# Optimization experiments

Measured on AMD Instinct MI355X. Metric: run time of the kernel, lower is better.

Reference implementation:

```python
import jax, jax.numpy as jnp
import numpy as np

GROUP = 4
ALPHA = 2.0


def sda(x, group=GROUP, alpha=ALPHA):
    # Per row: find FIRST group whose elements are all > 0 -> scale by alpha;
    # find FIRST group whose elements are all < 0 -> zero it. Masks are
    # computed on the original values, then applied.
    B, H = x.shape
    G = H // group
    xg = x.reshape(B, G, group)
    all_pos = jnp.all(xg > 0, axis=-1)            # [B, G]
    all_neg = jnp.all(xg < 0, axis=-1)            # [B, G]
    has_pos = jnp.any(all_pos, axis=-1, keepdims=True)   # [B, 1]
    has_neg = jnp.any(all_neg, axis=-1, keepdims=True)   # [B, 1]
    act_idx = jnp.argmax(all_pos, axis=-1, keepdims=True)    # first True
    inact_idx = jnp.argmax(all_neg, axis=-1, keepdims=True)  # first True
    gids = jnp.arange(G)[None, :]                 # [1, G]
    scale = jnp.ones((B, G), dtype=x.dtype)
    scale = jnp.where(has_pos & (gids == act_idx), jnp.asarray(alpha, x.dtype), scale)
    scale = jnp.where(has_neg & (gids == inact_idx), jnp.asarray(0.0, x.dtype), scale)
    return (xg * scale[:, :, None]).reshape(B, H)


def setup_inputs() -> dict:
    key = jax.random.key(0)
    ks = jax.random.split(key, 7)
    d_in, h1, h2, d_out = 1024, 4096, 4096, 1024
    x = jax.random.normal(ks[0], (8192, d_in), dtype=jnp.float32)
    def lin(kw, kb, fan_in, fan_out):
        bound = 1.0 / np.sqrt(fan_in)
        W = jax.random.uniform(kw, (fan_out, fan_in), jnp.float32, -bound, bound)
        b = jax.random.uniform(kb, (fan_out,), jnp.float32, -bound, bound)
        return W, b
    W1, b1 = lin(ks[1], ks[2], d_in, h1)
    W2, b2 = lin(ks[3], ks[4], h1, h2)
    W3, b3 = lin(ks[5], ks[6], h2, d_out)
    return {"x": x, "W1": W1, "b1": b1, "W2": W2, "b2": b2, "W3": W3, "b3": b3}


def reference(x, W1, b1, W2, b2, W3, b3):
    h = sda(x @ W1.T + b1)
    h = sda(h @ W2.T + b2)
    return h @ W3.T + b3
```

## Files before the change

kernel.cpp:

```cpp
#include <hip/hip_runtime.h>
#include <stdint.h>

using half8 = __attribute__((ext_vector_type(8))) _Float16;
using half4 = __attribute__((ext_vector_type(4))) _Float16;
using f32x4 = __attribute__((ext_vector_type(4))) float;

#define BM 256
#define BN 128
#define BK 32

__device__ __forceinline__ int swz(int row, int kb) {
  return (row << 6) + ((((kb >> 4) ^ ((row >> 1) & 3)) << 4) | (kb & 15));
}

__device__ __forceinline__ int xcd_swz(int bid, int nwg) {
  int cpx = nwg >> 3;
  return (bid & 7) * cpx + (bid >> 3);
}

#define GLD(src, dst)                                                          \
  __builtin_amdgcn_global_load_lds(                                            \
      (const __attribute__((address_space(1))) void*)(src),                    \
      (__attribute__((address_space(3))) void*)(dst), 16, 0, 0)

template <int MODE>
__global__ __launch_bounds__(1024, 4)
void gemm_tri(const _Float16* __restrict__ Ahi, const _Float16* __restrict__ Alo,
              const _Float16* __restrict__ Bhi, const _Float16* __restrict__ Blo,
              const float* __restrict__ bias,
              _Float16* __restrict__ Chi, _Float16* __restrict__ Clo,
              float* __restrict__ Cf, int M, int N, int K, int nbx) {
  constexpr bool LO = (MODE < 2);
  constexpr int AHI = 0;
  constexpr int ALO = 16384;
  constexpr int BHI = LO ? 32768 : 16384;
  constexpr int BLO = 40960;
  constexpr int STG = LO ? 49152 : 24576;
  __shared__ char lds[3 * STG];

  const int tid = threadIdx.x;
  const int sid = xcd_swz(blockIdx.x, gridDim.x);
  const int m0 = (sid / nbx) * BM;
  const int n0 = (sid % nbx) * BN;
  const int wave = tid >> 6, lane = tid & 63;
  const int wm = wave >> 1, wn = wave & 1;
  const int NK = K / BK;

  f32x4 acc_hi[2][4], acc_mid[2][4];
#pragma unroll
  for (int m = 0; m < 2; m++)
#pragma unroll
    for (int n = 0; n < 4; n++) { acc_hi[m][n] = (f32x4)0.0f; acc_mid[m][n] = (f32x4)0.0f; }

  const int srow = tid >> 2;
  const int kx = (tid & 3) ^ ((srow >> 1) & 3);
  const size_t aoff = (size_t)(m0 + srow) * K + kx * 8;
  const int brow = (tid & 511) >> 2;
  const size_t boff = (size_t)(n0 + brow) * K + kx * 8;

  auto STAGE = [&](int buf, int ks) {
    char* sb = lds + buf * STG;
    const size_t ko = (size_t)ks * BK;
    GLD(Ahi + aoff + ko, sb + AHI + (wave << 10));
    if constexpr (LO) {
      GLD(Alo + aoff + ko, sb + ALO + (wave << 10));
      if (wave < 8) GLD(Bhi + boff + ko, sb + BHI + (wave << 10));
      else          GLD(Blo + boff + ko, sb + BLO + ((wave - 8) << 10));
    } else {
      if (wave < 8) GLD(Bhi + boff + ko, sb + BHI + (wave << 10));
    }
  };

  auto COMPUTE = [&](int buf) {
    char* base = lds + buf * STG;
    const int kb = (lane >> 4) << 4;
    const int rl = lane & 15;
    half8 ah[2], al[2], bh[4], bl[4];
#pragma unroll
    for (int mi = 0; mi < 2; mi++) {
      int off = swz(wm * 32 + mi * 16 + rl, kb);
      ah[mi] = *(half8*)(base + AHI + off);
      if constexpr (LO) al[mi] = *(half8*)(base + ALO + off);
    }
#pragma unroll
    for (int ni = 0; ni < 4; ni++) {
      int off = swz(wn * 64 + ni * 16 + rl, kb);
      bh[ni] = *(half8*)(base + BHI + off);
      if constexpr (LO) bl[ni] = *(half8*)(base + BLO + off);
    }
    __builtin_amdgcn_s_setprio(1);
#pragma unroll
    for (int mi = 0; mi < 2; mi++)
#pragma unroll
      for (int ni = 0; ni < 4; ni++) {
        acc_hi[mi][ni] = __builtin_amdgcn_mfma_f32_16x16x32_f16(ah[mi], bh[ni], acc_hi[mi][ni], 0, 0, 0);
        if constexpr (LO) {
          acc_mid[mi][ni] = __builtin_amdgcn_mfma_f32_16x16x32_f16(ah[mi], bl[ni], acc_mid[mi][ni], 0, 0, 0);
          acc_mid[mi][ni] = __builtin_amdgcn_mfma_f32_16x16x32_f16(al[mi], bh[ni], acc_mid[mi][ni], 0, 0, 0);
        }
      }
    __builtin_amdgcn_s_setprio(0);
  };

  STAGE(0, 0);
  STAGE(1, 1);
  int cur = 0;
  for (int ks = 0; ks < NK; ++ks) {
    if (ks + 1 < NK) {
      if constexpr (LO) {
        asm volatile("s_waitcnt vmcnt(3)" ::: "memory");
      } else {
        if (wave < 8) asm volatile("s_waitcnt vmcnt(2)" ::: "memory");
        else          asm volatile("s_waitcnt vmcnt(1)" ::: "memory");
      }
    } else {
      asm volatile("s_waitcnt vmcnt(0)" ::: "memory");
    }
    __builtin_amdgcn_s_barrier();
    if (ks + 2 < NK) {
      int nbuf = cur + 2; if (nbuf >= 3) nbuf -= 3;
      STAGE(nbuf, ks + 2);
    }
    COMPUTE(cur);
    if (++cur == 3) cur = 0;
  }

  const int col_l = lane & 15, rgrp = lane >> 4;
#pragma unroll
  for (int ni = 0; ni < 4; ni++) {
    int col = n0 + wn * 64 + ni * 16 + col_l;
    float bv = bias[col];
#pragma unroll
    for (int mi = 0; mi < 2; mi++) {
      int rowb = m0 + wm * 32 + mi * 16 + rgrp * 4;
#pragma unroll
      for (int i = 0; i < 4; i++) {
        size_t idx = (size_t)(rowb + i) * N + col;
        if constexpr (MODE == 2) {
          Cf[idx] = acc_hi[mi][ni][i] + bv;
        } else {
          float c = acc_hi[mi][ni][i] + acc_mid[mi][ni][i] * (1.0f / 2048.0f) + bv;
          _Float16 hh = (_Float16)c;
          Chi[idx] = hh;
          if constexpr (MODE == 0) Clo[idx] = (_Float16)((c - (float)hh) * 2048.0f);
        }
      }
    }
  }
}

#define SQ_BUF 65536

__global__ __launch_bounds__(1024, 4)
void gemm_sq(const _Float16* __restrict__ Ahi, const _Float16* __restrict__ Bhi,
             const float* __restrict__ bias, _Float16* __restrict__ Chi,
             int M, int N, int K, int nbx) {
  __shared__ char lds[2 * SQ_BUF];
  const int tid = threadIdx.x;
  const int sid = xcd_swz(blockIdx.x, gridDim.x);
  const int m0 = (sid / nbx) * 256;
  const int n0 = (sid % nbx) * 256;
  const int wave = tid >> 6, lane = tid & 63;
  const int wm = wave >> 2, wn = wave & 3;
  const int NE = K / 64;

  f32x4 acc[4][4];
#pragma unroll
  for (int m = 0; m < 4; m++)
#pragma unroll
    for (int n = 0; n < 4; n++) acc[m][n] = (f32x4)0.0f;

  const int srow = tid >> 2;
  const int kx = (tid & 3) ^ ((srow >> 1) & 3);
  const size_t aoff = (size_t)(m0 + srow) * K + kx * 8;
  const size_t boff = (size_t)(n0 + srow) * K + kx * 8;

  const int kb = (lane >> 4) << 4;
  const int rl = lane & 15;
  int aswz[4], bswz[4];
#pragma unroll
  for (int i = 0; i < 4; i++) {
    aswz[i] = swz(wm * 64 + i * 16 + rl, kb);
    bswz[i] = 16384 + swz(wn * 64 + i * 16 + rl, kb);
  }

  auto STAGE_H = [&](int buf, int half, int ks) {
    char* sb = lds + buf * SQ_BUF + half * 32768 + (wave << 10);
    const size_t ko = (size_t)ks * BK;
    GLD(Ahi + aoff + ko, sb);
    GLD(Bhi + boff + ko, sb + 16384);
  };

  auto COMPUTE_H = [&](int buf, int half) {
    char* base = lds + buf * SQ_BUF + half * 32768;
    half8 ah[4], bh[4];
#pragma unroll
    for (int i = 0; i < 4; i++) {
      ah[i] = *(half8*)(base + aswz[i]);
      bh[i] = *(half8*)(base + bswz[i]);
    }
    __builtin_amdgcn_s_setprio(1);
#pragma unroll
    for (int mi = 0; mi < 4; mi++)
#pragma unroll
      for (int ni = 0; ni < 4; ni++)
        acc[mi][ni] = __builtin_amdgcn_mfma_f32_16x16x32_f16(ah[mi], bh[ni], acc[mi][ni], 0, 0, 0);
    __builtin_amdgcn_s_setprio(0);
  };

  STAGE_H(0, 0, 0);
  STAGE_H(0, 1, 1);
  int buf = 0;
  for (int e = 0; e < NE; ++e) {
    asm volatile("s_waitcnt vmcnt(0)" ::: "memory");
    __builtin_amdgcn_s_barrier();
    if (e + 1 < NE) STAGE_H(buf ^ 1, 0, 2 * e + 2);
    COMPUTE_H(buf, 0);
    if (e + 1 < NE) STAGE_H(buf ^ 1, 1, 2 * e + 3);
    COMPUTE_H(buf, 1);
    buf ^= 1;
  }

  const int col_l = lane & 15, rgrp = lane >> 4;
#pragma unroll
  for (int ni = 0; ni < 4; ni++) {
    int col = n0 + wn * 64 + ni * 16 + col_l;
    float bv = bias[col];
#pragma unroll
    for (int mi = 0; mi < 4; mi++) {
      int rowb = m0 + wm * 64 + mi * 16 + rgrp * 4;
#pragma unroll
      for (int i = 0; i < 4; i++)
        Chi[(size_t)(rowb + i) * N + col] = (_Float16)(acc[mi][ni][i] + bv);
    }
  }
}

__global__ __launch_bounds__(256)
void split4_kernel(const float* __restrict__ s0, _Float16* __restrict__ h0,
                   _Float16* __restrict__ l0, size_t n0,
                   const float* __restrict__ s1, _Float16* __restrict__ h1,
                   _Float16* __restrict__ l1, size_t n1,
                   const float* __restrict__ s2, _Float16* __restrict__ h2,
                   size_t n2,
                   const float* __restrict__ s3, _Float16* __restrict__ h3,
                   size_t n3) {
  const size_t tot = n0 + n1 + n2 + n3;
  size_t i = (size_t)blockIdx.x * 256 + threadIdx.x;
  const size_t stride = (size_t)gridDim.x * 256;
  for (; i < tot; i += stride) {
    const float* src; _Float16* hi; _Float16* lo; size_t j = i;
    if (j < n0) { src = s0; hi = h0; lo = l0; }
    else if ((j -= n0) < n1) { src = s1; hi = h1; lo = l1; }
    else if ((j -= n1) < n2) { src = s2; hi = h2; lo = nullptr; }
    else { j -= n2; src = s3; hi = h3; lo = nullptr; }
    float4 q = ((const float4*)src)[j];
    float a[4] = {q.x, q.y, q.z, q.w};
    half4 h, l;
#pragma unroll
    for (int k = 0; k < 4; ++k) {
      _Float16 hh = (_Float16)a[k];
      h[k] = hh;
      l[k] = (_Float16)((a[k] - (float)hh) * 2048.0f);
    }
    ((half4*)hi)[j] = h;
    if (lo) ((half4*)lo)[j] = l;
  }
}

__global__ __launch_bounds__(256)
void sda_fix(_Float16* __restrict__ Zhi, _Float16* __restrict__ Zlo,
             const float* __restrict__ Af,
             const _Float16* __restrict__ Ahi, const _Float16* __restrict__ Alo,
             const float* __restrict__ W, const float* __restrict__ bias,
             int H, int K, float TAU) {
  __shared__ int sPos[4], sNeg[4];
  __shared__ int nFix;
  __shared__ int fixIdx[96];
  __shared__ double sRed[4];
  __shared__ float sVal;
  const int row = blockIdx.x;
  _Float16* zh = Zhi + (size_t)row * H;
  _Float16* zl = Zlo ? Zlo + (size_t)row * H : nullptr;
  const int t = threadIdx.x;

  if (t == 0) nFix = 0;
  __syncthreads();

  float v[16];
  {
    half8 a0 = ((const half8*)zh)[t * 2], a1 = ((const half8*)zh)[t * 2 + 1];
    if (zl) {
      half8 b0 = ((const half8*)zl)[t * 2], b1 = ((const half8*)zl)[t * 2 + 1];
#pragma unroll
      for (int e = 0; e < 8; ++e) {
        v[e]     = (float)a0[e] + (float)b0[e] * (1.0f / 2048.0f);
        v[8 + e] = (float)a1[e] + (float)b1[e] * (1.0f / 2048.0f);
      }
    } else {
#pragma unroll
      for (int e = 0; e < 8; ++e) { v[e] = (float)a0[e]; v[8 + e] = (float)a1[e]; }
    }
  }

  bool cposa[4], pposa[4], cnega[4], pnega[4];
  int firstCpos = 0x7fffffff, firstCneg = 0x7fffffff;
#pragma unroll
  for (int j = 0; j < 4; ++j) {
    float g0 = v[j*4], g1 = v[j*4+1], g2 = v[j*4+2], g3 = v[j*4+3];
    cposa[j] = (g0 >  TAU) & (g1 >  TAU) & (g2 >  TAU) & (g3 >  TAU);
    pposa[j] = (g0 > -TAU) & (g1 > -TAU) & (g2 > -TAU) & (g3 > -TAU);
    cnega[j] = (g0 < -TAU) & (g1 < -TAU) & (g2 < -TAU) & (g3 < -TAU);
    pnega[j] = (g0 <  TAU) & (g1 <  TAU) & (g2 <  TAU) & (g3 <  TAU);
    int gi = (t << 2) + j;
    if (cposa[j] && gi < firstCpos) firstCpos = gi;
    if (cnega[j] && gi < firstCneg) firstCneg = gi;
  }
#pragma unroll
  for (int off = 32; off; off >>= 1) {
    firstCpos = min(firstCpos, __shfl_xor(firstCpos, off));
    firstCneg = min(firstCneg, __shfl_xor(firstCneg, off));
  }
  if ((t & 63) == 0) { sPos[t >> 6] = firstCpos; sNeg[t >> 6] = firstCneg; }
  __syncthreads();
  firstCpos = min(min(sPos[0], sPos[1]), min(sPos[2], sPos[3]));
  firstCneg = min(min(sNeg[0], sNeg[1]), min(sNeg[2], sNeg[3]));
  __syncthreads();

#pragma unroll
  for (int j = 0; j < 4; ++j) {
    int gi = (t << 2) + j;
    bool qual = (pposa[j] && !cposa[j] && gi <= firstCpos) ||
                (pnega[j] && !cnega[j] && gi <= firstCneg);
    if (qual) {
#pragma unroll
      for (int e = 0; e < 4; ++e) {
        if (fabsf(v[j*4+e]) < TAU) {
          int slot = atomicAdd(&nFix, 1);
          if (slot < 96) fixIdx[slot] = gi * 4 + e;
        }
      }
    }
  }
  __syncthreads();
  const int nf = min(nFix, 96);
  unsigned fixmask = 0;
  for (int i = 0; i < nf; ++i) {
    const int col = fixIdx[i];
    double s = 0.0;
    const float* wr = W + (size_t)col * K;
    if (Af) {
      const float* ar = Af + (size_t)row * K;
      for (int k = t; k < K; k += 256) s += (double)ar[k] * (double)wr[k];
    } else {
      const _Float16* ah = Ahi + (size_t)row * K;
      const _Float16* al = Alo + (size_t)row * K;
      for (int k = t; k < K; k += 256)
        s += ((double)(float)ah[k] + (double)(float)al[k] * (1.0 / 2048.0)) * (double)wr[k];
    }
#pragma unroll
    for (int off = 32; off; off >>= 1) s += __shfl_xor(s, off);
    if ((t & 63) == 0) sRed[t >> 6] = s;
    __syncthreads();
    if (t == 0)
      sVal = (float)(sRed[0] + sRed[1] + sRed[2] + sRed[3] + (double)bias[col]);
    __syncthreads();
    if ((col >> 4) == t) { v[col & 15] = sVal; fixmask |= 1u << (col & 15); }
    __syncthreads();
  }

  int fp = 0x7fffffff, fn = 0x7fffffff;
#pragma unroll
  for (int j = 0; j < 4; ++j) {
    bool ap = (v[j*4+0] > 0.f) & (v[j*4+1] > 0.f) & (v[j*4+2] > 0.f) & (v[j*4+3] > 0.f);
    bool an = (v[j*4+0] < 0.f) & (v[j*4+1] < 0.f) & (v[j*4+2] < 0.f) & (v[j*4+3] < 0.f);
    int g = (t << 2) + j;
    if (ap && g < fp) fp = g;
    if (an && g < fn) fn = g;
  }
#pragma unroll
  for (int off = 32; off; off >>= 1) {
    fp = min(fp, __shfl_xor(fp, off));
    fn = min(fn, __shfl_xor(fn, off));
  }
  if ((t & 63) == 0) { sPos[t >> 6] = fp; sNeg[t >> 6] = fn; }
  __syncthreads();
  fp = min(min(sPos[0], sPos[1]), min(sPos[2], sPos[3]));
  fn = min(min(sNeg[0], sNeg[1]), min(sNeg[2], sNeg[3]));
  const int act   = (fp == 0x7fffffff) ? -1 : fp;
  const int inact = (fn == 0x7fffffff) ? -1 : fn;

  unsigned chg = fixmask;
#pragma unroll
  for (int j = 0; j < 4; ++j) {
    int g = (t << 2) + j;
    if (g == act) {
      v[j*4+0] *= 2.f; v[j*4+1] *= 2.f; v[j*4+2] *= 2.f; v[j*4+3] *= 2.f;
      chg |= 0xFu << (j * 4);
    } else if (g == inact) {
      v[j*4+0] = v[j*4+1] = v[j*4+2] = v[j*4+3] = 0.f;
      chg |= 0xFu << (j * 4);
    }
  }
  while (chg) {
    int e = __ffs(chg) - 1; chg &= chg - 1;
    float val = v[e];
    _Float16 hh = (_Float16)val;
    zh[(t << 4) + e] = hh;
    if (zl) zl[(t << 4) + e] = (_Float16)((val - (float)hh) * 2048.0f);
  }
}

extern "C" void kernel_launch(void* const* d_in, const int* in_sizes, int n_in,
                              void* d_out, int out_size, void* d_ws, size_t ws_size,
                              hipStream_t stream) {
  const float* x  = (const float*)d_in[0];
  const float* W1 = (const float*)d_in[1];
  const float* b1 = (const float*)d_in[2];
  const float* W2 = (const float*)d_in[3];
  const float* b2 = (const float*)d_in[4];
  const float* W3 = (const float*)d_in[5];
  const float* b3 = (const float*)d_in[6];
  float* out = (float*)d_out;

  const int M = 8192, H = 4096, DIN = 1024, DOUT = 1024;

  char* w = (char*)d_ws;
  _Float16* Z1hi = (_Float16*)(w + 0);
  _Float16* Z1lo = (_Float16*)(w + ((size_t)64 << 20));
  _Float16* Z2hi = (_Float16*)(w + ((size_t)128 << 20));
  _Float16* W2hi = (_Float16*)(w + ((size_t)192 << 20));
  _Float16* xhi  = (_Float16*)(w + ((size_t)128 << 20));
  _Float16* xlo  = (_Float16*)(w + ((size_t)144 << 20));
  _Float16* W1hi = (_Float16*)(w + ((size_t)160 << 20));
  _Float16* W1lo = (_Float16*)(w + ((size_t)168 << 20));
  _Float16* W3hi = (_Float16*)(w + ((size_t)224 << 20));

  split4_kernel<<<2048, 256, 0, stream>>>(
      x,  xhi,  xlo,  (size_t)(M * DIN) >> 2,
      W1, W1hi, W1lo, (size_t)(H * DIN) >> 2,
      W2, W2hi,       (size_t)((size_t)H * H) >> 2,
      W3, W3hi,       (size_t)(DOUT * H) >> 2);

  gemm_tri<0><<<dim3((H / BN) * (M / BM)), dim3(1024), 0, stream>>>(
      xhi, xlo, W1hi, W1lo, b1, Z1hi, Z1lo, (float*)nullptr, M, H, DIN, H / BN);
  sda_fix<<<M, 256, 0, stream>>>(Z1hi, Z1lo, x, (const _Float16*)nullptr,
                                 (const _Float16*)nullptr, W1, b1, H, DIN, 1e-4f);
  gemm_sq<<<dim3((H / 256) * (M / 256)), dim3(1024), 0, stream>>>(
      Z1hi, W2hi, b2, Z2hi, M, H, H, H / 256);
  sda_fix<<<M, 256, 0, stream>>>(Z2hi, (_Float16*)nullptr, (const float*)nullptr,
                                 Z1hi, Z1lo, W2, b2, H, H, 5e-3f);
  gemm_tri<2><<<dim3((DOUT / BN) * (M / BM)), dim3(1024), 0, stream>>>(
      Z2hi, (const _Float16*)nullptr, W3hi, (const _Float16*)nullptr, b3,
      (_Float16*)nullptr, (_Float16*)nullptr, out, M, DOUT, H, DOUT / BN);
}
```

Before: 613.6 us.

## Load A operands directly from global into registers, stage only B in LDS

Both GEMM kernels stop staging the A tile through LDS. Each wave now loads its own A fragments straight from global memory into registers, and only B goes through LDS. The tri-split kernel drops from triple to double buffering with a full vmcnt(0) wait before every barrier. This cuts LDS footprint and LDS read traffic. In exchange it adds uncoalesced, strided global loads that stall the wave. A is no longer shared across the waves in the N direction (wn), so redundant global traffic rises.

```diff
diff --git a/kernel.cpp b/kernel.cpp
--- a/kernel.cpp
+++ b/kernel.cpp
@@ -31,12 +31,9 @@
               _Float16* __restrict__ Chi, _Float16* __restrict__ Clo,
               float* __restrict__ Cf, int M, int N, int K, int nbx) {
   constexpr bool LO = (MODE < 2);
-  constexpr int AHI = 0;
-  constexpr int ALO = 16384;
-  constexpr int BHI = LO ? 32768 : 16384;
-  constexpr int BLO = 40960;
-  constexpr int STG = LO ? 49152 : 24576;
-  __shared__ char lds[3 * STG];
+  constexpr int BLO = 8192;
+  constexpr int STG = LO ? 16384 : 8192;
+  __shared__ char lds[2 * STG];
 
   const int tid = threadIdx.x;
   const int sid = xcd_swz(blockIdx.x, gridDim.x);
@@ -52,41 +49,48 @@
 #pragma unroll
     for (int n = 0; n < 4; n++) { acc_hi[m][n] = (f32x4)0.0f; acc_mid[m][n] = (f32x4)0.0f; }
 
-  const int srow = tid >> 2;
-  const int kx = (tid & 3) ^ ((srow >> 1) & 3);
-  const size_t aoff = (size_t)(m0 + srow) * K + kx * 8;
   const int brow = (tid & 511) >> 2;
+  const int kx = (tid & 3) ^ ((brow >> 1) & 3);
   const size_t boff = (size_t)(n0 + brow) * K + kx * 8;
+
+  const int rl = lane & 15;
+  const int kb = (lane >> 4) << 4;
+  const _Float16* agp = Ahi + (size_t)(m0 + wm * 32 + rl) * K + ((lane >> 4) << 3);
+  const _Float16* agl = LO ? Alo + (size_t)(m0 + wm * 32 + rl) * K + ((lane >> 4) << 3)
+                           : nullptr;
+  const size_t aRowStride = (size_t)16 * K;
+
+  int bswz[4];
+#pragma unroll
+  for (int i = 0; i < 4; i++) bswz[i] = swz(wn * 64 + i * 16 + rl, kb);
 
   auto STAGE = [&](int buf, int ks) {
     char* sb = lds + buf * STG;
     const size_t ko = (size_t)ks * BK;
-    GLD(Ahi + aoff + ko, sb + AHI + (wave << 10));
     if constexpr (LO) {
-      GLD(Alo + aoff + ko, sb + ALO + (wave << 10));
-      if (wave < 8) GLD(Bhi + boff + ko, sb + BHI + (wave << 10));
+      if (wave < 8) GLD(Bhi + boff + ko, sb + (wave << 10));
       else          GLD(Blo + boff + ko, sb + BLO + ((wave - 8) << 10));
     } else {
-      if (wave < 8) GLD(Bhi + boff + ko, sb + BHI + (wave << 10));
-    }
-  };
-
-  auto COMPUTE = [&](int buf) {
+      if (wave < 8) GLD(Bhi + boff + ko, sb + (wave << 10));
+    }
+  };
+
+  auto LOAD_A = [&](half8 (&ah)[2], half8 (&al)[2], int ks) {
+    const size_t ko = (size_t)ks * BK;
+#pragma unroll
+    for (int mi = 0; mi < 2; mi++) {
+      ah[mi] = *(const half8*)(agp + ko + mi * aRowStride);
+      if constexpr (LO) al[mi] = *(const half8*)(agl + ko + mi * aRowStride);
+    }
+  };
+
+  auto COMPUTE = [&](int buf, half8 (&ah)[2], half8 (&al)[2]) {
     char* base = lds + buf * STG;
-    const int kb = (lane >> 4) << 4;
-    const int rl = lane & 15;
-    half8 ah[2], al[2], bh[4], bl[4];
-#pragma unroll
-    for (int mi = 0; mi < 2; mi++) {
-      int off = swz(wm * 32 + mi * 16 + rl, kb);
-      ah[mi] = *(half8*)(base + AHI + off);
-      if constexpr (LO) al[mi] = *(half8*)(base + ALO + off);
-    }
+    half8 bh[4], bl[4];
 #pragma unroll
     for (int ni = 0; ni < 4; ni++) {
-      int off = swz(wn * 64 + ni * 16 + rl, kb);
-      bh[ni] = *(half8*)(base + BHI + off);
-      if constexpr (LO) bl[ni] = *(half8*)(base + BLO + off);
+      bh[ni] = *(half8*)(base + bswz[ni]);
+      if constexpr (LO) bl[ni] = *(half8*)(base + BLO + bswz[ni]);
     }
     __builtin_amdgcn_s_setprio(1);
 #pragma unroll
@@ -102,27 +106,18 @@
     __builtin_amdgcn_s_setprio(0);
   };
 
+  half8 ahA[2], alA[2], ahB[2], alB[2];
+  LOAD_A(ahA, alA, 0);
   STAGE(0, 0);
-  STAGE(1, 1);
-  int cur = 0;
-  for (int ks = 0; ks < NK; ++ks) {
-    if (ks + 1 < NK) {
-      if constexpr (LO) {
-        asm volatile("s_waitcnt vmcnt(3)" ::: "memory");
-      } else {
-        if (wave < 8) asm volatile("s_waitcnt vmcnt(2)" ::: "memory");
-        else          asm volatile("s_waitcnt vmcnt(1)" ::: "memory");
-      }
-    } else {
-      asm volatile("s_waitcnt vmcnt(0)" ::: "memory");
-    }
+  for (int ks = 0; ks < NK; ks += 2) {
+    asm volatile("s_waitcnt vmcnt(0)" ::: "memory");
     __builtin_amdgcn_s_barrier();
-    if (ks + 2 < NK) {
-      int nbuf = cur + 2; if (nbuf >= 3) nbuf -= 3;
-      STAGE(nbuf, ks + 2);
-    }
-    COMPUTE(cur);
-    if (++cur == 3) cur = 0;
+    if (ks + 1 < NK) { STAGE(1, ks + 1); LOAD_A(ahB, alB, ks + 1); }
+    COMPUTE(0, ahA, alA);
+    asm volatile("s_waitcnt vmcnt(0)" ::: "memory");
+    __builtin_amdgcn_s_barrier();
+    if (ks + 2 < NK) { STAGE(0, ks + 2); LOAD_A(ahA, alA, ks + 2); }
+    COMPUTE(1, ahB, alB);
   }
 
   const int col_l = lane & 15, rgrp = lane >> 4;
@@ -149,7 +144,7 @@
   }
 }
 
-#define SQ_BUF 65536
+#define SQ_BUF 32768
 
 __global__ __launch_bounds__(1024, 4)
 void gemm_sq(const _Float16* __restrict__ Ahi, const _Float16* __restrict__ Bhi,
@@ -172,52 +167,54 @@
 
   const int srow = tid >> 2;
   const int kx = (tid & 3) ^ ((srow >> 1) & 3);
-  const size_t aoff = (size_t)(m0 + srow) * K + kx * 8;
   const size_t boff = (size_t)(n0 + srow) * K + kx * 8;
 
+  const int rl = lane & 15;
   const int kb = (lane >> 4) << 4;
-  const int rl = lane & 15;
-  int aswz[4], bswz[4];
-#pragma unroll
-  for (int i = 0; i < 4; i++) {
-    aswz[i] = swz(wm * 64 + i * 16 + rl, kb);
-    bswz[i] = 16384 + swz(wn * 64 + i * 16 + rl, kb);
-  }
-
-  auto STAGE_H = [&](int buf, int half, int ks) {
-    char* sb = lds + buf * SQ_BUF + half * 32768 + (wave << 10);
+  const _Float16* agp = Ahi + (size_t)(m0 + wm * 64 + rl) * K + ((lane >> 4) << 3);
+  const size_t aRowStride = (size_t)16 * K;
+
+  int bswz[4];
+#pragma unroll
+  for (int i = 0; i < 4; i++) bswz[i] = swz(wn * 64 + i * 16 + rl, kb);
+
+  auto STAGE_B = [&](int buf, int half, int ks) {
+    char* sb = lds + buf * SQ_BUF + half * 16384 + (wave << 10);
+    GLD(Bhi + boff + (size_t)ks * BK, sb);
+  };
+  auto LOAD_A = [&](half8 (&a)[4], int ks) {
     const size_t ko = (size_t)ks * BK;
-    GLD(Ahi + aoff + ko, sb);
-    GLD(Bhi + boff + ko, sb + 16384);
-  };
-
-  auto COMPUTE_H = [&](int buf, int half) {
-    char* base = lds + buf * SQ_BUF + half * 32768;
-    half8 ah[4], bh[4];
-#pragma unroll
-    for (int i = 0; i < 4; i++) {
-      ah[i] = *(half8*)(base + aswz[i]);
-      bh[i] = *(half8*)(base + bswz[i]);
-    }
+#pragma unroll
+    for (int mi = 0; mi < 4; mi++)
+      a[mi] = *(const half8*)(agp + ko + mi * aRowStride);
+  };
+  auto COMPUTE_H = [&](int buf, int half, half8 (&a)[4]) {
+    char* base = lds + buf * SQ_BUF + half * 16384;
+    half8 bh[4];
+#pragma unroll
+    for (int i = 0; i < 4; i++) bh[i] = *(half8*)(base + bswz[i]);
     __builtin_amdgcn_s_setprio(1);
 #pragma unroll
     for (int mi = 0; mi < 4; mi++)
 #pragma unroll
       for (int ni = 0; ni < 4; ni++)
-        acc[mi][ni] = __builtin_amdgcn_mfma_f32_16x16x32_f16(ah[mi], bh[ni], acc[mi][ni], 0, 0, 0);
+        acc[mi][ni] = __builtin_amdgcn_mfma_f32_16x16x32_f16(a[mi], bh[ni], acc[mi][ni], 0, 0, 0);
     __builtin_amdgcn_s_setprio(0);
   };
 
-  STAGE_H(0, 0, 0);
-  STAGE_H(0, 1, 1);
+  half8 a0[4], a1[4];
+  LOAD_A(a0, 0);
+  STAGE_B(0, 0, 0);
+  STAGE_B(0, 1, 1);
   int buf = 0;
   for (int e = 0; e < NE; ++e) {
     asm volatile("s_waitcnt vmcnt(0)" ::: "memory");
     __builtin_amdgcn_s_barrier();
-    if (e + 1 < NE) STAGE_H(buf ^ 1, 0, 2 * e + 2);
-    COMPUTE_H(buf, 0);
-    if (e + 1 < NE) STAGE_H(buf ^ 1, 1, 2 * e + 3);
-    COMPUTE_H(buf, 1);
+    if (e + 1 < NE) STAGE_B(buf ^ 1, 0, 2 * e + 2);
+    LOAD_A(a1, 2 * e + 1);
+    COMPUTE_H(buf, 0, a0);
+    if (e + 1 < NE) { STAGE_B(buf ^ 1, 1, 2 * e + 3); LOAD_A(a0, 2 * e + 2); }
+    COMPUTE_H(buf, 1, a1);
     buf ^= 1;
   }
 
```

After: 1.826 ms. 2.98x slower.
